# Kernel optimization log

Hardware: AMD Instinct MI355X
Metric: run time of the kernel (lower is better)

## Reference

```python
import jax, jax.numpy as jnp
import numpy as np

N_EXPERTS = 8
TOP_K = 2
D_MODEL = 1024
N_TOKENS = 8192


def setup_inputs() -> dict:
    key = jax.random.key(0)
    k1, k2, k3, k4, k5 = jax.random.split(key, 5)
    x = jax.random.normal(k1, (N_TOKENS, D_MODEL), dtype=jnp.float32)
    # router Linear(num_experts): weight [d, E], bias [E]
    Wr = jax.random.normal(k2, (D_MODEL, N_EXPERTS), dtype=jnp.float32) / np.sqrt(D_MODEL)
    br = jnp.zeros((N_EXPERTS,), dtype=jnp.float32)
    # per-expert Linear(d_model): stacked weights [E, d, d], biases [E, d]
    W = jax.random.normal(k3, (N_EXPERTS, D_MODEL, D_MODEL), dtype=jnp.float32) / np.sqrt(D_MODEL)
    b = jnp.zeros((N_EXPERTS, D_MODEL), dtype=jnp.float32)
    return {"x": x, "Wr": Wr, "br": br, "W": W, "b": b}


def reference(x, Wr, br, W, b):
    # --- route ---
    logits = x @ Wr + br                                  # [N, E]
    top_k_vals, top_k_idxs = jax.lax.top_k(logits, TOP_K)  # [N, k]
    top_k_gates = jax.nn.softmax(top_k_vals, axis=-1)      # [N, k]
    # --- experts (dense form of gather-dispatch; same math as routed compute) ---
    y_all = jnp.einsum('nd,edh->neh', x, W) + b            # [N, E, d]
    # --- gather routed expert outputs per slot ---
    y_k = jnp.take_along_axis(y_all, top_k_idxs[:, :, None], axis=1)  # [N, k, d]
    # --- weighted scatter-combine (reduce) ---
    out = jnp.sum(top_k_gates[:, :, None] * y_k, axis=1)   # [N, d]
    return out
```

## Files before the change

### kernel.cpp

```cpp
#include <hip/hip_runtime.h>
#include <hip/hip_bf16.h>


#define NTOK 8192
#define DM   1024
#define NEXP 8
#define CAP  8192
#define MAXT 136

typedef __attribute__((ext_vector_type(8))) short bf16x8;
typedef __attribute__((ext_vector_type(4))) float f32x4;

__device__ __forceinline__ unsigned short f2bf(float f) {
  unsigned u = __float_as_uint(f);
  unsigned r = (u + 0x7fffu + ((u >> 16) & 1u)) >> 16;
  return (unsigned short)r;
}
__device__ __forceinline__ float bf2f(unsigned short s) {
  return __uint_as_float(((unsigned)s) << 16);
}

__device__ __forceinline__ void gl_lds16(const void* g, void* l) {
  __builtin_amdgcn_global_load_lds(
      (const __attribute__((address_space(1))) unsigned int*)g,
      (__attribute__((address_space(3))) unsigned int*)l, 16, 0, 0);
}

__global__ __launch_bounds__(256) void transpose_w_kernel(
    const float* __restrict__ W, unsigned short* __restrict__ Wt) {
  __shared__ float tile[64][65];
  const int e = blockIdx.z;
  const int d0 = blockIdx.y * 64, h0 = blockIdx.x * 64;
  const float* Ws = W + (size_t)e * DM * DM;
  unsigned short* Wd = Wt + (size_t)e * DM * DM;
  const int r = threadIdx.x >> 4;
  const int c4 = (threadIdx.x & 15) * 4;
#pragma unroll
  for (int k = 0; k < 4; k++) {
    int row = r + k * 16;
    float4 v = *(const float4*)(Ws + (size_t)(d0 + row) * DM + h0 + c4);
    tile[row][c4 + 0] = v.x; tile[row][c4 + 1] = v.y;
    tile[row][c4 + 2] = v.z; tile[row][c4 + 3] = v.w;
  }
  __syncthreads();
#pragma unroll
  for (int k = 0; k < 4; k++) {
    int hrow = r + k * 16;
    ushort4 o;
    o.x = f2bf(tile[c4 + 0][hrow]);
    o.y = f2bf(tile[c4 + 1][hrow]);
    o.z = f2bf(tile[c4 + 2][hrow]);
    o.w = f2bf(tile[c4 + 3][hrow]);
    *(ushort4*)(Wd + (size_t)(h0 + hrow) * DM + d0 + c4) = o;
  }
}

__global__ __launch_bounds__(256) void router_compute_kernel(
    const float* __restrict__ x, const float* __restrict__ Wr,
    const float* __restrict__ br, unsigned short* __restrict__ xbf,
    int4* __restrict__ topk) {
  const int tid = threadIdx.x;
  const int wave = tid >> 6, lane = tid & 63;
  const int t = blockIdx.x * 4 + wave;
  const int c0 = lane * 16;
  const float* xr = x + (size_t)t * DM + c0;

  float v[16];
#pragma unroll
  for (int i = 0; i < 4; i++) {
    float4 f = *(const float4*)(xr + i * 4);
    v[i * 4 + 0] = f.x; v[i * 4 + 1] = f.y; v[i * 4 + 2] = f.z; v[i * 4 + 3] = f.w;
  }
  union { unsigned short s[8]; uint4 q; } pk;
#pragma unroll
  for (int half = 0; half < 2; half++) {
#pragma unroll
    for (int i = 0; i < 8; i++) pk.s[i] = f2bf(v[half * 8 + i]);
    *(uint4*)(xbf + (size_t)t * DM + c0 + half * 8) = pk.q;
  }
  float p[8] = {0, 0, 0, 0, 0, 0, 0, 0};
  const float* wr = Wr + (size_t)c0 * NEXP;
#pragma unroll
  for (int i = 0; i < 16; i++) {
    float xv = v[i];
    float4 wl = *(const float4*)(wr + i * 8);
    float4 wh = *(const float4*)(wr + i * 8 + 4);
    p[0] += xv * wl.x; p[1] += xv * wl.y; p[2] += xv * wl.z; p[3] += xv * wl.w;
    p[4] += xv * wh.x; p[5] += xv * wh.y; p[6] += xv * wh.z; p[7] += xv * wh.w;
  }
#pragma unroll
  for (int off = 32; off >= 1; off >>= 1) {
#pragma unroll
    for (int e = 0; e < 8; e++) p[e] += __shfl_xor(p[e], off, 64);
  }
  if (lane == 0) {
    float lg[8];
#pragma unroll
    for (int e = 0; e < 8; e++) lg[e] = p[e] + br[e];
    float v0 = lg[0]; int i0 = 0;
#pragma unroll
    for (int e = 1; e < 8; e++) if (lg[e] > v0) { v0 = lg[e]; i0 = e; }
    float v1 = -3.4e38f; int i1 = 0;
#pragma unroll
    for (int e = 0; e < 8; e++)
      if (e != i0 && lg[e] > v1) { v1 = lg[e]; i1 = e; }
    float ee = __expf(v1 - v0);
    float g0 = 1.0f / (1.0f + ee);
    float g1 = ee / (1.0f + ee);
    int4 rec;
    rec.x = i0; rec.y = i1;
    rec.z = __float_as_int(g0); rec.w = __float_as_int(g1);
    topk[t] = rec;
  }
}

__global__ __launch_bounds__(512) void scatter_kernel(
    const int4* __restrict__ topk, int* __restrict__ counts,
    int* __restrict__ tok, int2* __restrict__ pos) {
  __shared__ int lcnt[NEXP], lbase[NEXP];
  const int tid = threadIdx.x;
  if (tid < NEXP) lcnt[tid] = 0;
  __syncthreads();
  const int t = blockIdx.x * 512 + tid;
  int4 r = topk[t];
  int s0 = atomicAdd(&lcnt[r.x], 1);
  int s1 = atomicAdd(&lcnt[r.y], 1);
  __syncthreads();
  if (tid < NEXP) lbase[tid] = atomicAdd(&counts[tid], lcnt[tid]);
  __syncthreads();
  int p0 = lbase[r.x] + s0;
  int p1 = lbase[r.y] + s1;
  tok[r.x * CAP + p0] = t;
  tok[r.y * CAP + p1] = t;
  int2 pr; pr.x = p0; pr.y = p1;
  pos[t] = pr;
}

__global__ __launch_bounds__(64) void build_tiles_kernel(
    const int* __restrict__ counts, int* __restrict__ desc,
    int* __restrict__ ntiles, int* __restrict__ offset) {
  if (threadIdx.x == 0) {
    int idx = 0, off = 0;
#pragma unroll
    for (int e = 0; e < NEXP; e++) {
      offset[e] = off;
      off += counts[e];
      int nm = (counts[e] + 127) >> 7;
      for (int i = 0; i < nm; i++) desc[idx++] = (e << 16) | i;
    }
    *ntiles = idx;
  }
}

__global__ __launch_bounds__(256) void moe_gemm_kernel(
    const unsigned short* __restrict__ xbf, const unsigned short* __restrict__ wt,
    const int* __restrict__ counts, const int* __restrict__ offset,
    const int* __restrict__ tok, const int* __restrict__ desc,
    const int* __restrict__ ntiles, unsigned short* __restrict__ ybuf) {
  const int slot = blockIdx.y;
  if (slot >= *ntiles) return;
  const int dsc = desc[slot];
  const int e = dsc >> 16;
  const int m0 = (dsc & 0xffff) * 128;
  const int cnt = counts[e];
  const int n0 = blockIdx.x * 128;

  __shared__ __align__(16) unsigned short sA0[128 * 32];
  __shared__ __align__(16) unsigned short sB0[128 * 32];
  __shared__ __align__(16) unsigned short sA1[128 * 32];
  __shared__ __align__(16) unsigned short sB1[128 * 32];
  __shared__ int sTok[128];

  const int tid = threadIdx.x, wave = tid >> 6, lane = tid & 63;

  if (tid < 128) {
    int sr = m0 + tid;
    int cl = (sr < cnt) ? sr : (cnt - 1);
    sTok[tid] = tok[e * CAP + cl];
  }
  __syncthreads();

  const int rA1 = wave * 16 + (lane >> 2);
  const int rA2 = rA1 + 64;
  const int cch = lane & 3;
  const int cg1 = (cch ^ ((rA1 >> 1) & 3)) * 8;
  const int cg2 = (cch ^ ((rA2 >> 1) & 3)) * 8;
  const unsigned short* pA1 = xbf + (size_t)sTok[rA1] * DM + cg1;
  const unsigned short* pA2 = xbf + (size_t)sTok[rA2] * DM + cg2;
  const unsigned short* wte = wt + (size_t)e * DM * DM;
  const unsigned short* pB1 = wte + (size_t)(n0 + rA1) * DM + cg1;
  const unsigned short* pB2 = wte + (size_t)(n0 + rA2) * DM + cg2;
  const int lo1 = wave * 512, lo2 = (wave + 4) * 512;

  const int q = lane >> 4, ml = lane & 15;
  const int wm = (wave >> 1) * 64, wn = (wave & 1) * 64;
  int offA[4], offB[4];
#pragma unroll
  for (int i = 0; i < 4; i++) {
    int row = wm + i * 16 + ml;
    offA[i] = row * 32 + (q ^ ((row >> 1) & 3)) * 8;
    int rowb = wn + i * 16 + ml;
    offB[i] = rowb * 32 + (q ^ ((rowb >> 1) & 3)) * 8;
  }

  f32x4 acc[4][4] = {};

  for (int k0 = 0; k0 < DM; k0 += 64) {
    gl_lds16(pA1 + k0, sA0 + lo1);
    gl_lds16(pA2 + k0, sA0 + lo2);
    gl_lds16(pB1 + k0, sB0 + lo1);
    gl_lds16(pB2 + k0, sB0 + lo2);
    gl_lds16(pA1 + k0 + 32, sA1 + lo1);
    gl_lds16(pA2 + k0 + 32, sA1 + lo2);
    gl_lds16(pB1 + k0 + 32, sB1 + lo1);
    gl_lds16(pB2 + k0 + 32, sB1 + lo2);
    __syncthreads();
    bf16x8 af0[4], bf0[4], af1[4], bf1[4];
#pragma unroll
    for (int i = 0; i < 4; i++) {
      af0[i] = *(const bf16x8*)(sA0 + offA[i]);
      bf0[i] = *(const bf16x8*)(sB0 + offB[i]);
      af1[i] = *(const bf16x8*)(sA1 + offA[i]);
      bf1[i] = *(const bf16x8*)(sB1 + offB[i]);
    }
#pragma unroll
    for (int mt = 0; mt < 4; mt++)
#pragma unroll
      for (int nt = 0; nt < 4; nt++)
        acc[mt][nt] = __builtin_amdgcn_mfma_f32_16x16x32_bf16(
            af0[mt], bf0[nt], acc[mt][nt], 0, 0, 0);
#pragma unroll
    for (int mt = 0; mt < 4; mt++)
#pragma unroll
      for (int nt = 0; nt < 4; nt++)
        acc[mt][nt] = __builtin_amdgcn_mfma_f32_16x16x32_bf16(
            af1[mt], bf1[nt], acc[mt][nt], 0, 0, 0);
    __syncthreads();
  }

  const int yb = offset[e] + m0;
#pragma unroll
  for (int mt = 0; mt < 4; mt++) {
    int rbase = wm + mt * 16 + q * 4;
#pragma unroll
    for (int r = 0; r < 4; r++) {
      int row = rbase + r;
      if (m0 + row >= cnt) continue;
      unsigned short* yrow = ybuf + (size_t)(yb + row) * DM + n0;
#pragma unroll
      for (int nt = 0; nt < 4; nt++) {
        yrow[wn + nt * 16 + ml] = f2bf(acc[mt][nt][r]);
      }
    }
  }
}

__global__ __launch_bounds__(256) void combine_kernel(
    const unsigned short* __restrict__ ybuf, const int4* __restrict__ topk,
    const int2* __restrict__ pos, const int* __restrict__ offset,
    const float* __restrict__ bias, float* __restrict__ out) {
  const int t = blockIdx.x;
  const int c = threadIdx.x * 4;
  int4 r = topk[t];
  int2 p = pos[t];
  float g0 = __int_as_float(r.z), g1 = __int_as_float(r.w);
  int s0 = offset[r.x] + p.x;
  int s1 = offset[r.y] + p.y;
  ushort4 ya = *(const ushort4*)(ybuf + (size_t)s0 * DM + c);
  ushort4 yb = *(const ushort4*)(ybuf + (size_t)s1 * DM + c);
  float4 b0 = *(const float4*)(bias + (size_t)r.x * DM + c);
  float4 b1 = *(const float4*)(bias + (size_t)r.y * DM + c);
  float4 o;
  o.x = g0 * (bf2f(ya.x) + b0.x) + g1 * (bf2f(yb.x) + b1.x);
  o.y = g0 * (bf2f(ya.y) + b0.y) + g1 * (bf2f(yb.y) + b1.y);
  o.z = g0 * (bf2f(ya.z) + b0.z) + g1 * (bf2f(yb.z) + b1.z);
  o.w = g0 * (bf2f(ya.w) + b0.w) + g1 * (bf2f(yb.w) + b1.w);
  *(float4*)(out + (size_t)t * DM + c) = o;
}

extern "C" void kernel_launch(void* const* d_in, const int* in_sizes, int n_in,
                              void* d_out, int out_size, void* d_ws, size_t ws_size,
                              hipStream_t stream) {
  const float* x  = (const float*)d_in[0];
  const float* Wr = (const float*)d_in[1];
  const float* br = (const float*)d_in[2];
  const float* W  = (const float*)d_in[3];
  const float* b  = (const float*)d_in[4];
  float* out = (float*)d_out;

  char* ws = (char*)d_ws;
  unsigned short* xbf  = (unsigned short*)ws;
  unsigned short* wt   = (unsigned short*)(ws + (16u << 20));
  unsigned short* ybuf = (unsigned short*)(ws + (32u << 20));
  char* ctrl = ws + (64u << 20);
  int*   counts = (int*)ctrl;
  int*   ntiles = (int*)(ctrl + 64);
  int*   offset = (int*)(ctrl + 128);
  int*   desc   = (int*)(ctrl + 256);
  int*   tok    = (int*)(ctrl + 4096);
  int2*  pos    = (int2*)(ctrl + 4096 + (256u << 10));
  int4*  topk   = (int4*)(ctrl + 4096 + (320u << 10));

  hipMemsetAsync(counts, 0, 128, stream);

  transpose_w_kernel<<<dim3(16, 16, 8), 256, 0, stream>>>(W, wt);
  router_compute_kernel<<<NTOK / 4, 256, 0, stream>>>(x, Wr, br, xbf, topk);
  scatter_kernel<<<16, 512, 0, stream>>>(topk, counts, tok, pos);
  build_tiles_kernel<<<1, 64, 0, stream>>>(counts, desc, ntiles, offset);
  moe_gemm_kernel<<<dim3(8, MAXT), 256, 0, stream>>>(
      xbf, wt, counts, offset, tok, desc, ntiles, ybuf);
  combine_kernel<<<NTOK, 256, 0, stream>>>(ybuf, topk, pos, offset, b, out);
}
```

Before: 214.5 us.

## Fuse weight transpose, routing, scatter and tile build into one prep kernel

Merges the weight transpose/convert, router, scatter and tile-descriptor kernels into a single launch. Blocks are split by index into transpose and routing roles, and the last routing block, found with an atomic done-counter, builds the tile descriptors. The transpose and routing work can now overlap and three launches disappear. The combine kernel now handles four tokens per block. Risks: each routing block processes 64 tokens serially across its waves, which lowers parallelism for the router, and the last-block pattern relies on threadfence ordering.

New measurement: 211.6 us. About the same (-1.3%).

```diff
diff --git a/kernel.cpp b/kernel.cpp
--- a/kernel.cpp
+++ b/kernel.cpp
@@ -8,6 +8,9 @@
 #define CAP  8192
 #define MAXT 136
 
+#define TRB  2048
+#define RTB  128
+
 typedef __attribute__((ext_vector_type(8))) short bf16x8;
 typedef __attribute__((ext_vector_type(4))) float f32x4;
 
@@ -26,129 +29,154 @@
       (__attribute__((address_space(3))) unsigned int*)l, 16, 0, 0);
 }
 
-__global__ __launch_bounds__(256) void transpose_w_kernel(
-    const float* __restrict__ W, unsigned short* __restrict__ Wt) {
-  __shared__ float tile[64][65];
-  const int e = blockIdx.z;
-  const int d0 = blockIdx.y * 64, h0 = blockIdx.x * 64;
-  const float* Ws = W + (size_t)e * DM * DM;
-  unsigned short* Wd = Wt + (size_t)e * DM * DM;
-  const int r = threadIdx.x >> 4;
-  const int c4 = (threadIdx.x & 15) * 4;
-#pragma unroll
-  for (int k = 0; k < 4; k++) {
-    int row = r + k * 16;
-    float4 v = *(const float4*)(Ws + (size_t)(d0 + row) * DM + h0 + c4);
-    tile[row][c4 + 0] = v.x; tile[row][c4 + 1] = v.y;
-    tile[row][c4 + 2] = v.z; tile[row][c4 + 3] = v.w;
-  }
-  __syncthreads();
-#pragma unroll
-  for (int k = 0; k < 4; k++) {
-    int hrow = r + k * 16;
-    ushort4 o;
-    o.x = f2bf(tile[c4 + 0][hrow]);
-    o.y = f2bf(tile[c4 + 1][hrow]);
-    o.z = f2bf(tile[c4 + 2][hrow]);
-    o.w = f2bf(tile[c4 + 3][hrow]);
-    *(ushort4*)(Wd + (size_t)(h0 + hrow) * DM + d0 + c4) = o;
-  }
-}
-
-__global__ __launch_bounds__(256) void router_compute_kernel(
+__global__ __launch_bounds__(256) void prep_kernel(
+    const float* __restrict__ W, unsigned short* __restrict__ Wt,
     const float* __restrict__ x, const float* __restrict__ Wr,
     const float* __restrict__ br, unsigned short* __restrict__ xbf,
-    int4* __restrict__ topk) {
+    int4* __restrict__ topk, int* __restrict__ counts,
+    int* __restrict__ tok, int2* __restrict__ pos,
+    int* __restrict__ done, int* __restrict__ desc,
+    int* __restrict__ ntiles, int* __restrict__ offset) {
+  __shared__ __align__(16) float smem[64 * 65];
   const int tid = threadIdx.x;
+
+  if (blockIdx.x < TRB) {
+    float (*tile)[65] = (float(*)[65])smem;
+    const int e = blockIdx.x >> 8;
+    const int rem = blockIdx.x & 255;
+    const int d0 = (rem >> 4) * 64, h0 = (rem & 15) * 64;
+    const float* Ws = W + (size_t)e * DM * DM;
+    unsigned short* Wd = Wt + (size_t)e * DM * DM;
+    const int r = tid >> 4;
+    const int c4 = (tid & 15) * 4;
+#pragma unroll
+    for (int k = 0; k < 4; k++) {
+      int row = r + k * 16;
+      float4 v = *(const float4*)(Ws + (size_t)(d0 + row) * DM + h0 + c4);
+      tile[row][c4 + 0] = v.x; tile[row][c4 + 1] = v.y;
+      tile[row][c4 + 2] = v.z; tile[row][c4 + 3] = v.w;
+    }
+    __syncthreads();
+#pragma unroll
+    for (int k = 0; k < 4; k++) {
+      int hrow = r + k * 16;
+      ushort4 o;
+      o.x = f2bf(tile[c4 + 0][hrow]);
+      o.y = f2bf(tile[c4 + 1][hrow]);
+      o.z = f2bf(tile[c4 + 2][hrow]);
+      o.w = f2bf(tile[c4 + 3][hrow]);
+      *(ushort4*)(Wd + (size_t)(h0 + hrow) * DM + d0 + c4) = o;
+    }
+    return;
+  }
+
+  int*  lcnt  = (int*)smem;
+  int4* ltop  = (int4*)(smem + 16);
+  int2* lrank = (int2*)(smem + 16 + 256);
+
+  const int rb = blockIdx.x - TRB;
   const int wave = tid >> 6, lane = tid & 63;
-  const int t = blockIdx.x * 4 + wave;
+  const int tbase = rb * 64;
+  if (tid < NEXP) lcnt[tid] = 0;
+
   const int c0 = lane * 16;
-  const float* xr = x + (size_t)t * DM + c0;
-
-  float v[16];
-#pragma unroll
-  for (int i = 0; i < 4; i++) {
-    float4 f = *(const float4*)(xr + i * 4);
-    v[i * 4 + 0] = f.x; v[i * 4 + 1] = f.y; v[i * 4 + 2] = f.z; v[i * 4 + 3] = f.w;
-  }
-  union { unsigned short s[8]; uint4 q; } pk;
-#pragma unroll
-  for (int half = 0; half < 2; half++) {
-#pragma unroll
-    for (int i = 0; i < 8; i++) pk.s[i] = f2bf(v[half * 8 + i]);
-    *(uint4*)(xbf + (size_t)t * DM + c0 + half * 8) = pk.q;
-  }
-  float p[8] = {0, 0, 0, 0, 0, 0, 0, 0};
   const float* wr = Wr + (size_t)c0 * NEXP;
-#pragma unroll
-  for (int i = 0; i < 16; i++) {
-    float xv = v[i];
-    float4 wl = *(const float4*)(wr + i * 8);
-    float4 wh = *(const float4*)(wr + i * 8 + 4);
-    p[0] += xv * wl.x; p[1] += xv * wl.y; p[2] += xv * wl.z; p[3] += xv * wl.w;
-    p[4] += xv * wh.x; p[5] += xv * wh.y; p[6] += xv * wh.z; p[7] += xv * wh.w;
-  }
-#pragma unroll
-  for (int off = 32; off >= 1; off >>= 1) {
-#pragma unroll
-    for (int e = 0; e < 8; e++) p[e] += __shfl_xor(p[e], off, 64);
-  }
-  if (lane == 0) {
-    float lg[8];
-#pragma unroll
-    for (int e = 0; e < 8; e++) lg[e] = p[e] + br[e];
-    float v0 = lg[0]; int i0 = 0;
-#pragma unroll
-    for (int e = 1; e < 8; e++) if (lg[e] > v0) { v0 = lg[e]; i0 = e; }
-    float v1 = -3.4e38f; int i1 = 0;
-#pragma unroll
-    for (int e = 0; e < 8; e++)
-      if (e != i0 && lg[e] > v1) { v1 = lg[e]; i1 = e; }
-    float ee = __expf(v1 - v0);
-    float g0 = 1.0f / (1.0f + ee);
-    float g1 = ee / (1.0f + ee);
-    int4 rec;
-    rec.x = i0; rec.y = i1;
-    rec.z = __float_as_int(g0); rec.w = __float_as_int(g1);
-    topk[t] = rec;
-  }
-}
-
-__global__ __launch_bounds__(512) void scatter_kernel(
-    const int4* __restrict__ topk, int* __restrict__ counts,
-    int* __restrict__ tok, int2* __restrict__ pos) {
-  __shared__ int lcnt[NEXP], lbase[NEXP];
-  const int tid = threadIdx.x;
-  if (tid < NEXP) lcnt[tid] = 0;
-  __syncthreads();
-  const int t = blockIdx.x * 512 + tid;
-  int4 r = topk[t];
-  int s0 = atomicAdd(&lcnt[r.x], 1);
-  int s1 = atomicAdd(&lcnt[r.y], 1);
-  __syncthreads();
-  if (tid < NEXP) lbase[tid] = atomicAdd(&counts[tid], lcnt[tid]);
-  __syncthreads();
-  int p0 = lbase[r.x] + s0;
-  int p1 = lbase[r.y] + s1;
-  tok[r.x * CAP + p0] = t;
-  tok[r.y * CAP + p1] = t;
-  int2 pr; pr.x = p0; pr.y = p1;
-  pos[t] = pr;
-}
-
-__global__ __launch_bounds__(64) void build_tiles_kernel(
-    const int* __restrict__ counts, int* __restrict__ desc,
-    int* __restrict__ ntiles, int* __restrict__ offset) {
-  if (threadIdx.x == 0) {
-    int idx = 0, off = 0;
-#pragma unroll
-    for (int e = 0; e < NEXP; e++) {
-      offset[e] = off;
-      off += counts[e];
-      int nm = (counts[e] + 127) >> 7;
-      for (int i = 0; i < nm; i++) desc[idx++] = (e << 16) | i;
-    }
-    *ntiles = idx;
+
+#pragma unroll 1
+  for (int it = 0; it < 16; it++) {
+    const int t = tbase + wave * 16 + it;
+    const float* xr = x + (size_t)t * DM + c0;
+    float v[16];
+#pragma unroll
+    for (int i = 0; i < 4; i++) {
+      float4 f = *(const float4*)(xr + i * 4);
+      v[i * 4 + 0] = f.x; v[i * 4 + 1] = f.y;
+      v[i * 4 + 2] = f.z; v[i * 4 + 3] = f.w;
+    }
+    union { unsigned short s[8]; uint4 q; } pk;
+#pragma unroll
+    for (int half = 0; half < 2; half++) {
+#pragma unroll
+      for (int i = 0; i < 8; i++) pk.s[i] = f2bf(v[half * 8 + i]);
+      *(uint4*)(xbf + (size_t)t * DM + c0 + half * 8) = pk.q;
+    }
+    float p[8] = {0, 0, 0, 0, 0, 0, 0, 0};
+#pragma unroll
+    for (int i = 0; i < 16; i++) {
+      float xv = v[i];
+      float4 wl = *(const float4*)(wr + i * 8);
+      float4 wh = *(const float4*)(wr + i * 8 + 4);
+      p[0] += xv * wl.x; p[1] += xv * wl.y; p[2] += xv * wl.z; p[3] += xv * wl.w;
+      p[4] += xv * wh.x; p[5] += xv * wh.y; p[6] += xv * wh.z; p[7] += xv * wh.w;
+    }
+#pragma unroll
+    for (int off = 32; off >= 1; off >>= 1) {
+#pragma unroll
+      for (int e = 0; e < 8; e++) p[e] += __shfl_xor(p[e], off, 64);
+    }
+    if (lane == 0) {
+      float lg[8];
+#pragma unroll
+      for (int e = 0; e < 8; e++) lg[e] = p[e] + br[e];
+      float v0 = lg[0]; int i0 = 0;
+#pragma unroll
+      for (int e = 1; e < 8; e++) if (lg[e] > v0) { v0 = lg[e]; i0 = e; }
+      float v1 = -3.4e38f; int i1 = 0;
+#pragma unroll
+      for (int e = 0; e < 8; e++)
+        if (e != i0 && lg[e] > v1) { v1 = lg[e]; i1 = e; }
+      float ee = __expf(v1 - v0);
+      float g0 = 1.0f / (1.0f + ee);
+      float g1 = ee / (1.0f + ee);
+      int4 rec;
+      rec.x = i0; rec.y = i1;
+      rec.z = __float_as_int(g0); rec.w = __float_as_int(g1);
+      ltop[wave * 16 + it] = rec;
+      topk[t] = rec;
+    }
+  }
+  __syncthreads();
+
+  if (tid < 64) {
+    int4 r = ltop[tid];
+    int s0 = atomicAdd(&lcnt[r.x], 1);
+    int s1 = atomicAdd(&lcnt[r.y], 1);
+    int2 rk; rk.x = s0; rk.y = s1;
+    lrank[tid] = rk;
+  }
+  __syncthreads();
+  if (tid < NEXP) lcnt[tid] = atomicAdd(&counts[tid], lcnt[tid]);
+  __syncthreads();
+  if (tid < 64) {
+    int4 r = ltop[tid];
+    int2 rk = lrank[tid];
+    int p0 = lcnt[r.x] + rk.x;
+    int p1 = lcnt[r.y] + rk.y;
+    int t = tbase + tid;
+    tok[r.x * CAP + p0] = t;
+    tok[r.y * CAP + p1] = t;
+    int2 pr; pr.x = p0; pr.y = p1;
+    pos[t] = pr;
+  }
+  __syncthreads();
+
+  if (tid == 0) {
+    __threadfence();
+    if (atomicAdd(done, 1) == RTB - 1) {
+      __threadfence();
+      int cnt[NEXP];
+#pragma unroll
+      for (int e = 0; e < NEXP; e++) cnt[e] = atomicAdd(&counts[e], 0);
+      int idx = 0, off = 0;
+#pragma unroll
+      for (int e = 0; e < NEXP; e++) {
+        offset[e] = off;
+        off += cnt[e];
+        int nm = (cnt[e] + 127) >> 7;
+        for (int i = 0; i < nm; i++) desc[idx++] = (e << 16) | i;
+      }
+      *ntiles = idx;
+    }
   }
 }
 
@@ -259,23 +287,27 @@
     const unsigned short* __restrict__ ybuf, const int4* __restrict__ topk,
     const int2* __restrict__ pos, const int* __restrict__ offset,
     const float* __restrict__ bias, float* __restrict__ out) {
-  const int t = blockIdx.x;
   const int c = threadIdx.x * 4;
-  int4 r = topk[t];
-  int2 p = pos[t];
-  float g0 = __int_as_float(r.z), g1 = __int_as_float(r.w);
-  int s0 = offset[r.x] + p.x;
-  int s1 = offset[r.y] + p.y;
-  ushort4 ya = *(const ushort4*)(ybuf + (size_t)s0 * DM + c);
-  ushort4 yb = *(const ushort4*)(ybuf + (size_t)s1 * DM + c);
-  float4 b0 = *(const float4*)(bias + (size_t)r.x * DM + c);
-  float4 b1 = *(const float4*)(bias + (size_t)r.y * DM + c);
-  float4 o;
-  o.x = g0 * (bf2f(ya.x) + b0.x) + g1 * (bf2f(yb.x) + b1.x);
-  o.y = g0 * (bf2f(ya.y) + b0.y) + g1 * (bf2f(yb.y) + b1.y);
-  o.z = g0 * (bf2f(ya.z) + b0.z) + g1 * (bf2f(yb.z) + b1.z);
-  o.w = g0 * (bf2f(ya.w) + b0.w) + g1 * (bf2f(yb.w) + b1.w);
-  *(float4*)(out + (size_t)t * DM + c) = o;
+  const int t0 = blockIdx.x * 4;
+#pragma unroll
+  for (int i = 0; i < 4; i++) {
+    const int t = t0 + i;
+    int4 r = topk[t];
+    int2 p = pos[t];
+    float g0 = __int_as_float(r.z), g1 = __int_as_float(r.w);
+    int s0 = offset[r.x] + p.x;
+    int s1 = offset[r.y] + p.y;
+    ushort4 ya = *(const ushort4*)(ybuf + (size_t)s0 * DM + c);
+    ushort4 yb = *(const ushort4*)(ybuf + (size_t)s1 * DM + c);
+    float4 b0 = *(const float4*)(bias + (size_t)r.x * DM + c);
+    float4 b1 = *(const float4*)(bias + (size_t)r.y * DM + c);
+    float4 o;
+    o.x = g0 * (bf2f(ya.x) + b0.x) + g1 * (bf2f(yb.x) + b1.x);
+    o.y = g0 * (bf2f(ya.y) + b0.y) + g1 * (bf2f(yb.y) + b1.y);
+    o.z = g0 * (bf2f(ya.z) + b0.z) + g1 * (bf2f(yb.z) + b1.z);
+    o.w = g0 * (bf2f(ya.w) + b0.w) + g1 * (bf2f(yb.w) + b1.w);
+    *(float4*)(out + (size_t)t * DM + c) = o;
+  }
 }
 
 extern "C" void kernel_launch(void* const* d_in, const int* in_sizes, int n_in,
@@ -295,19 +327,18 @@
   char* ctrl = ws + (64u << 20);
   int*   counts = (int*)ctrl;
   int*   ntiles = (int*)(ctrl + 64);
+  int*   done   = (int*)(ctrl + 96);
   int*   offset = (int*)(ctrl + 128);
   int*   desc   = (int*)(ctrl + 256);
   int*   tok    = (int*)(ctrl + 4096);
   int2*  pos    = (int2*)(ctrl + 4096 + (256u << 10));
   int4*  topk   = (int4*)(ctrl + 4096 + (320u << 10));
 
-  hipMemsetAsync(counts, 0, 128, stream);
-
-  transpose_w_kernel<<<dim3(16, 16, 8), 256, 0, stream>>>(W, wt);
-  router_compute_kernel<<<NTOK / 4, 256, 0, stream>>>(x, Wr, br, xbf, topk);
-  scatter_kernel<<<16, 512, 0, stream>>>(topk, counts, tok, pos);
-  build_tiles_kernel<<<1, 64, 0, stream>>>(counts, desc, ntiles, offset);
+  hipMemsetAsync(ctrl, 0, 128, stream);
+
+  prep_kernel<<<TRB + RTB, 256, 0, stream>>>(
+      W, wt, x, Wr, br, xbf, topk, counts, tok, pos, done, desc, ntiles, offset);
   moe_gemm_kernel<<<dim3(8, MAXT), 256, 0, stream>>>(
       xbf, wt, counts, offset, tok, desc, ntiles, ybuf);
-  combine_kernel<<<NTOK, 256, 0, stream>>>(ybuf, topk, pos, offset, b, out);
-}
+  combine_kernel<<<NTOK / 4, 256, 0, stream>>>(ybuf, topk, pos, offset, b, out);
+}
```
